# Performance work log

Measured on AMD Instinct MI355X. Metric: run time of the kernel, lower is better.

## Reference

```python
import jax, jax.numpy as jnp
import numpy as np

NUM_STAGES = 2
DE_NEIGHBORS = 3

def _square_distance(a, b):
    # a: [B,N,3], b: [B,S,3] -> [B,N,S] squared euclidean distances
    return (jnp.sum(a * a, axis=-1)[:, :, None]
            + jnp.sum(b * b, axis=-1)[:, None, :]
            - 2.0 * jnp.einsum('bnc,bsc->bns', a, b))

def _propagate(xyz1, xyz2, points1, points2, k):
    # xyz1:[B,N,3] fine, xyz2:[B,S,3] coarse, points1:[B,D1,N], points2:[B,D2,S]
    p2 = jnp.transpose(points2, (0, 2, 1))  # [B,S,D2]
    B, N, _ = xyz1.shape
    S = xyz2.shape[1]
    if S == 1:
        interp = jnp.broadcast_to(p2, (B, N, p2.shape[-1]))
    else:
        d = _square_distance(xyz1, xyz2)              # [B,N,S]
        neg_top, idx = jax.lax.top_k(-d, k)           # k smallest distances
        dists = -neg_top                              # [B,N,k]
        recip = 1.0 / (dists + 1e-8)
        weight = recip / jnp.sum(recip, axis=2, keepdims=True)  # [B,N,k]
        # gather neighbor features: [B,N,k,D2]
        gathered = jnp.take_along_axis(p2[:, None, :, :], idx[..., None], axis=2)
        interp = jnp.sum(gathered * weight[..., None], axis=2)  # [B,N,D2]
    if points1 is not None:
        p1 = jnp.transpose(points1, (0, 2, 1))        # [B,N,D1]
        new = jnp.concatenate([p1, interp], axis=-1)
    else:
        new = interp
    return jnp.transpose(new, (0, 2, 1))              # [B,D1+D2,N]

def setup_inputs() -> dict:
    key = jax.random.key(0)
    ks = jax.random.split(key, 6)
    return {
        'xyz0': jax.random.normal(ks[0], (4, 8192, 3), dtype=jnp.float32),
        'xyz1': jax.random.normal(ks[1], (4, 2048, 3), dtype=jnp.float32),
        'xyz2': jax.random.normal(ks[2], (4, 512, 3), dtype=jnp.float32),
        'x0': jax.random.normal(ks[3], (4, 128, 8192), dtype=jnp.float32),
        'x1': jax.random.normal(ks[4], (4, 256, 2048), dtype=jnp.float32),
        'x2': jax.random.normal(ks[5], (4, 512, 512), dtype=jnp.float32),
    }

def reference(xyz0, xyz1, xyz2, x0, x1, x2):
    # original forward reverses the lists; emulate with pre-reversed lists
    xyz_list = [xyz2, xyz1, xyz0]   # coarse -> fine
    x_list = [x2, x1, x0]
    x = x_list[0]
    for i in range(NUM_STAGES):
        x = _propagate(xyz_list[i + 1], xyz_list[i], x_list[i + 1], x, DE_NEIGHBORS)
    return x  # [4, 896, 8192]
```

## Files before the change

kernel.cpp:

```cpp
#include <hip/hip_runtime.h>

#define BIG 3.0e38f

typedef float vf4 __attribute__((ext_vector_type(4)));

__device__ __forceinline__ void insert3(float d, int s,
                                        float& d0, float& d1, float& d2,
                                        int& i0, int& i1, int& i2) {
    const bool b0 = d < d0;
    const bool b1 = d < d1;
    const bool b2 = d < d2;
    i2 = b1 ? i1 : (b2 ? s : i2);
    i1 = b0 ? i0 : (b1 ? s : i1);
    i0 = b0 ? s  : i0;
    const float nd1 = __builtin_amdgcn_fmed3f(d, d0, d1);
    d2 = __builtin_amdgcn_fmed3f(d, d1, d2);
    d0 = fminf(d, d0);
    d1 = nd1;
}

template <int S>
__device__ void knn_tile(const float* __restrict__ xyzF, const float* __restrict__ xyzC,
                         int N, int b, int nb,
                         int* __restrict__ idx, float* __restrict__ w,
                         void* smem) {
    constexpr int SPC = S / 8;
    float4* sc  = (float4*)smem;
    float*  smd = (float*)((char*)smem + S * 16);
    int*    smi = (int*)((char*)smem + S * 16 + 3072);
    const int tid = threadIdx.x;

    for (int i = tid; i < S; i += 256) {
        const float x = xyzC[(b * S + i) * 3 + 0];
        const float y = xyzC[(b * S + i) * 3 + 1];
        const float z = xyzC[(b * S + i) * 3 + 2];
        sc[i] = make_float4(x, y, z, x * x + y * y + z * z);
    }
    __syncthreads();

    const int q  = tid & 31;
    const int sp = tid >> 5;
    const int n  = nb + q;
    const float ax = xyzF[(b * N + n) * 3 + 0];
    const float ay = xyzF[(b * N + n) * 3 + 1];
    const float az = xyzF[(b * N + n) * 3 + 2];
    const float an = ax * ax + ay * ay + az * az;

    float d0 = BIG, d1 = BIG, d2 = BIG;
    int i0 = 0, i1 = 0, i2 = 0;
    const int s0 = sp * SPC;
#pragma unroll 8
    for (int s = s0; s < s0 + SPC; ++s) {
        const float4 p = sc[s];
        const float t = ax * p.x + ay * p.y + az * p.z;
        const float d = an + p.w - 2.0f * t;
        insert3(d, s, d0, d1, d2, i0, i1, i2);
    }

    smd[tid * 3 + 0] = d0; smi[tid * 3 + 0] = i0;
    smd[tid * 3 + 1] = d1; smi[tid * 3 + 1] = i1;
    smd[tid * 3 + 2] = d2; smi[tid * 3 + 2] = i2;
    __syncthreads();

    if (tid < 32) {
        float e0 = BIG, e1 = BIG, e2 = BIG;
        int j0 = 0, j1 = 0, j2 = 0;
#pragma unroll
        for (int ch = 0; ch < 8; ++ch) {
#pragma unroll
            for (int k = 0; k < 3; ++k) {
                insert3(smd[(ch * 32 + tid) * 3 + k], smi[(ch * 32 + tid) * 3 + k],
                        e0, e1, e2, j0, j1, j2);
            }
        }
        const float r0 = 1.0f / (e0 + 1e-8f);
        const float r1 = 1.0f / (e1 + 1e-8f);
        const float r2 = 1.0f / (e2 + 1e-8f);
        const float rs = r0 + r1 + r2;
        const int nn = nb + tid;
        idx[(b * 3 + 0) * N + nn] = j0;
        idx[(b * 3 + 1) * N + nn] = j1;
        idx[(b * 3 + 2) * N + nn] = j2;
        w[(b * 3 + 0) * N + nn] = r0 / rs;
        w[(b * 3 + 1) * N + nn] = r1 / rs;
        w[(b * 3 + 2) * N + nn] = r2 / rs;
    }
}

__device__ void transpose_tile(const float* __restrict__ in, float* __restrict__ out,
                               int C, int N, int OS,
                               int b, int nb, int cb, void* smem) {
    float (*s)[65] = (float (*)[65])smem;
    const int lo = threadIdx.x & 63;
    const int r  = threadIdx.x >> 6;
#pragma unroll
    for (int i = 0; i < 16; ++i) {
        const int cl = r + 4 * i;
        s[cl][lo] = in[((size_t)b * C + cb + cl) * N + nb + lo];
    }
    __syncthreads();
#pragma unroll
    for (int i = 0; i < 16; ++i) {
        const int pl = r + 4 * i;
        out[((size_t)b * N + nb + pl) * OS + cb + lo] = s[lo][pl];
    }
}

__global__ __launch_bounds__(256) void k1_stage(const float* __restrict__ xyz0,
                                                const float* __restrict__ xyz1,
                                                const float* __restrict__ xyz2,
                                                const float* __restrict__ x0,
                                                const float* __restrict__ x1,
                                                const float* __restrict__ x2,
                                                float* __restrict__ x1P,
                                                float* __restrict__ x2P,
                                                int* __restrict__ idx1,
                                                float* __restrict__ w1,
                                                int* __restrict__ idx2,
                                                float* __restrict__ w2,
                                                float* __restrict__ out) {
    __shared__ float4 smem4[2432];
    const int id = blockIdx.x;
    if (id < 1024) {
        const int b  = id >> 8;
        const int nb = (id & 255) * 32;
        knn_tile<2048>(xyz0, xyz1, 8192, b, nb, idx2, w2, smem4);
    } else if (id < 1280) {
        const int r  = id - 1024;
        const int b  = r >> 6;
        const int nb = (r & 63) * 32;
        knn_tile<512>(xyz1, xyz2, 2048, b, nb, idx1, w1, smem4);
    } else if (id < 1536) {
        const int r  = id - 1280;
        const int b  = r >> 6;
        const int nb = (r & 7) * 64;
        const int cb = ((r >> 3) & 7) * 64;
        transpose_tile(x2, x2P, 512, 512, 512, b, nb, cb, smem4);
    } else if (id < 2048) {
        const int r  = id - 1536;
        const int b  = r >> 7;
        const int nb = (r & 31) * 64;
        const int cb = ((r >> 5) & 3) * 64;
        transpose_tile(x1, x1P, 256, 2048, 256, b, nb, cb, smem4);
    } else {
        const int r  = id - 2048;
        const int b  = r >> 6;
        const int lb = r & 63;
        const vf4* src = (const vf4*)x0;
        vf4* dst = (vf4*)out;
#pragma unroll
        for (int t = 0; t < 16; ++t) {
            const int i = lb * 4096 + t * 256 + threadIdx.x;
            const vf4 v = __builtin_nontemporal_load(&src[(size_t)b * (128 * 2048) + i]);
            __builtin_nontemporal_store(v, &dst[(size_t)b * (896 * 2048) + i]);
        }
    }
}

__global__ __launch_bounds__(256) void final_unified(const float* __restrict__ x1P,
                                                     const float* __restrict__ x2P,
                                                     const int* __restrict__ idx1,
                                                     const float* __restrict__ w1,
                                                     const int* __restrict__ idx2,
                                                     const float* __restrict__ w2,
                                                     float* __restrict__ out) {
    __shared__ float tile[64][65];
    __shared__ int   sj1[3][64];
    __shared__ float sw1[3][64];
    __shared__ int   sj9[9][64];
    __shared__ float sw9[9][64];
    const int id  = blockIdx.x;
    const int xcd = id & 7;
    const int b   = xcd >> 1;
    const int ntile = ((id >> 3) << 1) | (xcd & 1);
    const int nb  = ntile * 64;
    const int tid = threadIdx.x;

    if (tid < 192) {
        const int p = tid & 63, k = tid >> 6;
        const int   j  = idx2[(b * 3 + k) * 8192 + nb + p];
        const float wk = w2[(b * 3 + k) * 8192 + nb + p];
        sj1[k][p] = j * 256;
        sw1[k][p] = wk;
#pragma unroll
        for (int m = 0; m < 3; ++m) {
            sj9[k * 3 + m][p] = idx1[(b * 3 + m) * 2048 + j] * 512;
            sw9[k * 3 + m][p] = wk * w1[(b * 3 + m) * 2048 + j];
        }
    }
    __syncthreads();

    const int c = tid & 63;
    const int r = tid >> 6;

    for (int ct = 0; ct < 4; ++ct) {
        const int cb = ct * 64;
        const float* xb = x1P + (size_t)b * 2048 * 256 + cb + c;
#pragma unroll 8
        for (int i = 0; i < 16; ++i) {
            const int p = r + 4 * i;
            tile[p][c] = sw1[0][p] * xb[sj1[0][p]]
                       + sw1[1][p] * xb[sj1[1][p]]
                       + sw1[2][p] * xb[sj1[2][p]];
        }
        __syncthreads();
        {
            const int p = tid & 63;
#pragma unroll
            for (int i = 0; i < 16; ++i) {
                const int cl = r + 4 * i;
                __builtin_nontemporal_store(tile[p][cl],
                    &out[((size_t)b * 896 + 128 + cb + cl) * 8192 + nb + p]);
            }
        }
        __syncthreads();
    }

    for (int ct = 0; ct < 8; ++ct) {
        const int cb = ct * 64;
        const float* xb = x2P + (size_t)b * 512 * 512 + cb + c;
#pragma unroll 4
        for (int i = 0; i < 16; ++i) {
            const int p = r + 4 * i;
            float v = 0.0f;
#pragma unroll
            for (int j = 0; j < 9; ++j) {
                v += sw9[j][p] * xb[sj9[j][p]];
            }
            tile[p][c] = v;
        }
        __syncthreads();
        {
            const int p = tid & 63;
#pragma unroll
            for (int i = 0; i < 16; ++i) {
                const int cl = r + 4 * i;
                __builtin_nontemporal_store(tile[p][cl],
                    &out[((size_t)b * 896 + 384 + cb + cl) * 8192 + nb + p]);
            }
        }
        __syncthreads();
    }
}

extern "C" void kernel_launch(void* const* d_in, const int* in_sizes, int n_in,
                              void* d_out, int out_size, void* d_ws, size_t ws_size,
                              hipStream_t stream) {
    const float* xyz0 = (const float*)d_in[0];
    const float* xyz1 = (const float*)d_in[1];
    const float* xyz2 = (const float*)d_in[2];
    const float* x0   = (const float*)d_in[3];
    const float* x1   = (const float*)d_in[4];
    const float* x2   = (const float*)d_in[5];
    float* out = (float*)d_out;

    char* ws = (char*)d_ws;
    float* x1P  = (float*)(ws + 0);
    float* x2P  = (float*)(ws + 8388608);
    int*   idx1 = (int*)(ws + 12582912);
    float* w1   = (float*)(ws + 12681216);
    int*   idx2 = (int*)(ws + 12779520);
    float* w2   = (float*)(ws + 13172736);

    k1_stage<<<dim3(2304), 256, 0, stream>>>(xyz0, xyz1, xyz2, x0, x1, x2,
                                             x1P, x2P, idx1, w1, idx2, w2, out);
    final_unified<<<dim3(512), 256, 0, stream>>>(x1P, x2P, idx1, w1, idx2, w2, out);
}
```

Baseline: 248.9 us.

## Rebalance work across two kernels with vectorized gathers and phased KNN tiles

Moves the x0 copy out of the first kernel into the second, so the first kernel only does KNN and transposes. The final gather kernel is split into many more independent blocks: the stage-2 gathers are spread over two channel halves per tile and the stage-1 gathers over one 64-channel slab each, and both now use float4 vector loads. The KNN is split into two phases over half of the coarse points to cut shared memory, and the distance uses a half-norm FMA form with the query norm added back at the end. A tie-breaking merge is used for the final top-3 selection. Together these aim at higher occupancy and better load balance, at the cost of recomputing the neighbor index and weight setup in every block and an extra barrier per KNN phase.

```diff
diff --git a/kernel.cpp b/kernel.cpp
--- a/kernel.cpp
+++ b/kernel.cpp
@@ -3,6 +3,8 @@
 #define BIG 3.0e38f
 
 typedef float vf4 __attribute__((ext_vector_type(4)));
+
+__device__ __forceinline__ vf4 ld4(const float* p) { return *(const vf4*)p; }
 
 __device__ __forceinline__ void insert3(float d, int s,
                                         float& d0, float& d1, float& d2,
@@ -19,42 +21,58 @@
     d1 = nd1;
 }
 
-template <int S>
+__device__ __forceinline__ void insert3_tie(float d, int s,
+                                            float& d0, float& d1, float& d2,
+                                            int& i0, int& i1, int& i2) {
+    const bool b0 = (d < d0) | ((d == d0) & (s < i0));
+    const bool b1 = (d < d1) | ((d == d1) & (s < i1));
+    const bool b2 = (d < d2) | ((d == d2) & (s < i2));
+    i2 = b1 ? i1 : (b2 ? s : i2);
+    i1 = b0 ? i0 : (b1 ? s : i1);
+    i0 = b0 ? s  : i0;
+    d2 = b1 ? d1 : (b2 ? d : d2);
+    d1 = b0 ? d0 : (b1 ? d : d1);
+    d0 = b0 ? d  : d0;
+}
+
+template <int S, int PHASES>
 __device__ void knn_tile(const float* __restrict__ xyzF, const float* __restrict__ xyzC,
                          int N, int b, int nb,
                          int* __restrict__ idx, float* __restrict__ w,
                          void* smem) {
-    constexpr int SPC = S / 8;
+    constexpr int H   = S / PHASES;
+    constexpr int SPC = H / 8;
     float4* sc  = (float4*)smem;
-    float*  smd = (float*)((char*)smem + S * 16);
-    int*    smi = (int*)((char*)smem + S * 16 + 3072);
+    float*  smd = (float*)((char*)smem + H * 16);
+    int*    smi = (int*)((char*)smem + H * 16 + 3072);
     const int tid = threadIdx.x;
-
-    for (int i = tid; i < S; i += 256) {
-        const float x = xyzC[(b * S + i) * 3 + 0];
-        const float y = xyzC[(b * S + i) * 3 + 1];
-        const float z = xyzC[(b * S + i) * 3 + 2];
-        sc[i] = make_float4(x, y, z, x * x + y * y + z * z);
-    }
-    __syncthreads();
-
-    const int q  = tid & 31;
-    const int sp = tid >> 5;
-    const int n  = nb + q;
+    const int q   = tid & 31;
+    const int sp  = tid >> 5;
+    const int n   = nb + q;
     const float ax = xyzF[(b * N + n) * 3 + 0];
     const float ay = xyzF[(b * N + n) * 3 + 1];
     const float az = xyzF[(b * N + n) * 3 + 2];
-    const float an = ax * ax + ay * ay + az * az;
 
     float d0 = BIG, d1 = BIG, d2 = BIG;
     int i0 = 0, i1 = 0, i2 = 0;
-    const int s0 = sp * SPC;
+
+    for (int ph = 0; ph < PHASES; ++ph) {
+        const int base = ph * H;
+        if (ph) __syncthreads();
+        for (int i = tid; i < H; i += 256) {
+            const float x = xyzC[(b * S + base + i) * 3 + 0];
+            const float y = xyzC[(b * S + base + i) * 3 + 1];
+            const float z = xyzC[(b * S + base + i) * 3 + 2];
+            sc[i] = make_float4(x, y, z, 0.5f * (x * x + y * y + z * z));
+        }
+        __syncthreads();
+        const int s0 = sp * SPC;
 #pragma unroll 8
-    for (int s = s0; s < s0 + SPC; ++s) {
-        const float4 p = sc[s];
-        const float t = ax * p.x + ay * p.y + az * p.z;
-        const float d = an + p.w - 2.0f * t;
-        insert3(d, s, d0, d1, d2, i0, i1, i2);
+        for (int t = 0; t < SPC; ++t) {
+            const float4 p = sc[s0 + t];
+            const float h = fmaf(-ax, p.x, fmaf(-ay, p.y, fmaf(-az, p.z, p.w)));
+            insert3(h, base + s0 + t, d0, d1, d2, i0, i1, i2);
+        }
     }
 
     smd[tid * 3 + 0] = d0; smi[tid * 3 + 0] = i0;
@@ -69,13 +87,14 @@
         for (int ch = 0; ch < 8; ++ch) {
 #pragma unroll
             for (int k = 0; k < 3; ++k) {
-                insert3(smd[(ch * 32 + tid) * 3 + k], smi[(ch * 32 + tid) * 3 + k],
-                        e0, e1, e2, j0, j1, j2);
-            }
-        }
-        const float r0 = 1.0f / (e0 + 1e-8f);
-        const float r1 = 1.0f / (e1 + 1e-8f);
-        const float r2 = 1.0f / (e2 + 1e-8f);
+                insert3_tie(smd[(ch * 32 + tid) * 3 + k], smi[(ch * 32 + tid) * 3 + k],
+                            e0, e1, e2, j0, j1, j2);
+            }
+        }
+        const float an = ax * ax + ay * ay + az * az;
+        const float r0 = 1.0f / (fmaf(2.0f, e0, an) + 1e-8f);
+        const float r1 = 1.0f / (fmaf(2.0f, e1, an) + 1e-8f);
+        const float r2 = 1.0f / (fmaf(2.0f, e2, an) + 1e-8f);
         const float rs = r0 + r1 + r2;
         const int nn = nb + tid;
         idx[(b * 3 + 0) * N + nn] = j0;
@@ -109,7 +128,6 @@
 __global__ __launch_bounds__(256) void k1_stage(const float* __restrict__ xyz0,
                                                 const float* __restrict__ xyz1,
                                                 const float* __restrict__ xyz2,
-                                                const float* __restrict__ x0,
                                                 const float* __restrict__ x1,
                                                 const float* __restrict__ x2,
                                                 float* __restrict__ x1P,
@@ -117,129 +135,144 @@
                                                 int* __restrict__ idx1,
                                                 float* __restrict__ w1,
                                                 int* __restrict__ idx2,
-                                                float* __restrict__ w2,
-                                                float* __restrict__ out) {
-    __shared__ float4 smem4[2432];
+                                                float* __restrict__ w2) {
+    __shared__ float4 smem4[1408];
     const int id = blockIdx.x;
     if (id < 1024) {
         const int b  = id >> 8;
         const int nb = (id & 255) * 32;
-        knn_tile<2048>(xyz0, xyz1, 8192, b, nb, idx2, w2, smem4);
+        knn_tile<2048, 2>(xyz0, xyz1, 8192, b, nb, idx2, w2, smem4);
     } else if (id < 1280) {
         const int r  = id - 1024;
         const int b  = r >> 6;
         const int nb = (r & 63) * 32;
-        knn_tile<512>(xyz1, xyz2, 2048, b, nb, idx1, w1, smem4);
+        knn_tile<512, 1>(xyz1, xyz2, 2048, b, nb, idx1, w1, smem4);
     } else if (id < 1536) {
         const int r  = id - 1280;
         const int b  = r >> 6;
         const int nb = (r & 7) * 64;
         const int cb = ((r >> 3) & 7) * 64;
         transpose_tile(x2, x2P, 512, 512, 512, b, nb, cb, smem4);
-    } else if (id < 2048) {
+    } else {
         const int r  = id - 1536;
         const int b  = r >> 7;
         const int nb = (r & 31) * 64;
         const int cb = ((r >> 5) & 3) * 64;
         transpose_tile(x1, x1P, 256, 2048, 256, b, nb, cb, smem4);
+    }
+}
+
+__global__ __launch_bounds__(256) void k2_final(const float* __restrict__ x0,
+                                                const float* __restrict__ x1P,
+                                                const float* __restrict__ x2P,
+                                                const int* __restrict__ idx1,
+                                                const float* __restrict__ w1,
+                                                const int* __restrict__ idx2,
+                                                const float* __restrict__ w2,
+                                                float* __restrict__ out) {
+    __shared__ vf4 smemv[1376];
+    float (*tile)[68] = (float (*)[68])smemv;
+    int*   sj9 = (int*)((float*)smemv + 4352);
+    float* sw9 = (float*)((float*)smemv + 4928);
+    const int id  = blockIdx.x;
+    const int tid = threadIdx.x;
+    const int q4  = tid & 15;
+    const int pg  = (tid >> 4) & 3;
+    const int r   = tid >> 6;
+
+    if (id < 1024) {
+        const int b     = id >> 8;
+        const int rem   = id & 255;
+        const int ntile = rem >> 1;
+        const int cq    = rem & 1;
+        const int nb    = ntile * 64;
+
+        if (tid < 192) {
+            const int p = tid & 63, k = tid >> 6;
+            const int   j  = idx2[(b * 3 + k) * 8192 + nb + p];
+            const float wk = w2[(b * 3 + k) * 8192 + nb + p];
+#pragma unroll
+            for (int m = 0; m < 3; ++m) {
+                sj9[(k * 3 + m) * 64 + p] = idx1[(b * 3 + m) * 2048 + j] * 512;
+                sw9[(k * 3 + m) * 64 + p] = wk * w1[(b * 3 + m) * 2048 + j];
+            }
+        }
+        __syncthreads();
+
+        for (int ct = 0; ct < 4; ++ct) {
+            const int cb = (cq * 4 + ct) * 64;
+            const float* xb = x2P + (size_t)b * 512 * 512 + cb + q4 * 4;
+#pragma unroll
+            for (int i = 0; i < 4; ++i) {
+                const int p = i * 16 + r * 4 + pg;
+                vf4 acc = sw9[0 * 64 + p] * ld4(xb + sj9[0 * 64 + p]);
+#pragma unroll
+                for (int j = 1; j < 9; ++j) {
+                    acc += sw9[j * 64 + p] * ld4(xb + sj9[j * 64 + p]);
+                }
+                *(vf4*)&tile[p][q4 * 4] = acc;
+            }
+            __syncthreads();
+            {
+                const int p2 = tid & 63;
+#pragma unroll
+                for (int i = 0; i < 16; ++i) {
+                    const int cl = r + 4 * i;
+                    __builtin_nontemporal_store(tile[p2][cl],
+                        &out[((size_t)b * 896 + 384 + cb + cl) * 8192 + nb + p2]);
+                }
+            }
+            __syncthreads();
+        }
+    } else if (id < 3072) {
+        const int t     = id - 1024;
+        const int b     = t >> 9;
+        const int rem   = t & 511;
+        const int ntile = rem >> 2;
+        const int ct    = rem & 3;
+        const int nb    = ntile * 64;
+        const int cb    = ct * 64;
+        int*   sj1 = sj9;
+        float* sw1 = sw9;
+
+        if (tid < 192) {
+            const int p = tid & 63, k = tid >> 6;
+            sj1[k * 64 + p] = idx2[(b * 3 + k) * 8192 + nb + p] * 256;
+            sw1[k * 64 + p] = w2[(b * 3 + k) * 8192 + nb + p];
+        }
+        __syncthreads();
+
+        const float* xb = x1P + (size_t)b * 2048 * 256 + cb + q4 * 4;
+#pragma unroll
+        for (int i = 0; i < 4; ++i) {
+            const int p = i * 16 + r * 4 + pg;
+            const vf4 acc = sw1[0 * 64 + p] * ld4(xb + sj1[0 * 64 + p])
+                          + sw1[1 * 64 + p] * ld4(xb + sj1[1 * 64 + p])
+                          + sw1[2 * 64 + p] * ld4(xb + sj1[2 * 64 + p]);
+            *(vf4*)&tile[p][q4 * 4] = acc;
+        }
+        __syncthreads();
+        {
+            const int p2 = tid & 63;
+#pragma unroll
+            for (int i = 0; i < 16; ++i) {
+                const int cl = r + 4 * i;
+                __builtin_nontemporal_store(tile[p2][cl],
+                    &out[((size_t)b * 896 + 128 + cb + cl) * 8192 + nb + p2]);
+            }
+        }
     } else {
-        const int r  = id - 2048;
-        const int b  = r >> 6;
-        const int lb = r & 63;
+        const int rr = id - 3072;
+        const int b  = rr >> 6;
+        const int lb = rr & 63;
         const vf4* src = (const vf4*)x0;
         vf4* dst = (vf4*)out;
 #pragma unroll
-        for (int t = 0; t < 16; ++t) {
-            const int i = lb * 4096 + t * 256 + threadIdx.x;
+        for (int t2 = 0; t2 < 16; ++t2) {
+            const int i = lb * 4096 + t2 * 256 + tid;
             const vf4 v = __builtin_nontemporal_load(&src[(size_t)b * (128 * 2048) + i]);
             __builtin_nontemporal_store(v, &dst[(size_t)b * (896 * 2048) + i]);
         }
-    }
-}
-
-__global__ __launch_bounds__(256) void final_unified(const float* __restrict__ x1P,
-                                                     const float* __restrict__ x2P,
-                                                     const int* __restrict__ idx1,
-                                                     const float* __restrict__ w1,
-                                                     const int* __restrict__ idx2,
-                                                     const float* __restrict__ w2,
-                                                     float* __restrict__ out) {
-    __shared__ float tile[64][65];
-    __shared__ int   sj1[3][64];
-    __shared__ float sw1[3][64];
-    __shared__ int   sj9[9][64];
-    __shared__ float sw9[9][64];
-    const int id  = blockIdx.x;
-    const int xcd = id & 7;
-    const int b   = xcd >> 1;
-    const int ntile = ((id >> 3) << 1) | (xcd & 1);
-    const int nb  = ntile * 64;
-    const int tid = threadIdx.x;
-
-    if (tid < 192) {
-        const int p = tid & 63, k = tid >> 6;
-        const int   j  = idx2[(b * 3 + k) * 8192 + nb + p];
-        const float wk = w2[(b * 3 + k) * 8192 + nb + p];
-        sj1[k][p] = j * 256;
-        sw1[k][p] = wk;
-#pragma unroll
-        for (int m = 0; m < 3; ++m) {
-            sj9[k * 3 + m][p] = idx1[(b * 3 + m) * 2048 + j] * 512;
-            sw9[k * 3 + m][p] = wk * w1[(b * 3 + m) * 2048 + j];
-        }
-    }
-    __syncthreads();
-
-    const int c = tid & 63;
-    const int r = tid >> 6;
-
-    for (int ct = 0; ct < 4; ++ct) {
-        const int cb = ct * 64;
-        const float* xb = x1P + (size_t)b * 2048 * 256 + cb + c;
-#pragma unroll 8
-        for (int i = 0; i < 16; ++i) {
-            const int p = r + 4 * i;
-            tile[p][c] = sw1[0][p] * xb[sj1[0][p]]
-                       + sw1[1][p] * xb[sj1[1][p]]
-                       + sw1[2][p] * xb[sj1[2][p]];
-        }
-        __syncthreads();
-        {
-            const int p = tid & 63;
-#pragma unroll
-            for (int i = 0; i < 16; ++i) {
-                const int cl = r + 4 * i;
-                __builtin_nontemporal_store(tile[p][cl],
-                    &out[((size_t)b * 896 + 128 + cb + cl) * 8192 + nb + p]);
-            }
-        }
-        __syncthreads();
-    }
-
-    for (int ct = 0; ct < 8; ++ct) {
-        const int cb = ct * 64;
-        const float* xb = x2P + (size_t)b * 512 * 512 + cb + c;
-#pragma unroll 4
-        for (int i = 0; i < 16; ++i) {
-            const int p = r + 4 * i;
-            float v = 0.0f;
-#pragma unroll
-            for (int j = 0; j < 9; ++j) {
-                v += sw9[j][p] * xb[sj9[j][p]];
-            }
-            tile[p][c] = v;
-        }
-        __syncthreads();
-        {
-            const int p = tid & 63;
-#pragma unroll
-            for (int i = 0; i < 16; ++i) {
-                const int cl = r + 4 * i;
-                __builtin_nontemporal_store(tile[p][cl],
-                    &out[((size_t)b * 896 + 384 + cb + cl) * 8192 + nb + p]);
-            }
-        }
-        __syncthreads();
     }
 }
 
@@ -262,7 +295,7 @@
     int*   idx2 = (int*)(ws + 12779520);
     float* w2   = (float*)(ws + 13172736);
 
-    k1_stage<<<dim3(2304), 256, 0, stream>>>(xyz0, xyz1, xyz2, x0, x1, x2,
-                                             x1P, x2P, idx1, w1, idx2, w2, out);
-    final_unified<<<dim3(512), 256, 0, stream>>>(x1P, x2P, idx1, w1, idx2, w2, out);
-}
+    k1_stage<<<dim3(2048), 256, 0, stream>>>(xyz0, xyz1, xyz2, x1, x2,
+                                             x1P, x2P, idx1, w1, idx2, w2);
+    k2_final<<<dim3(3328), 256, 0, stream>>>(x0, x1P, x2P, idx1, w1, idx2, w2, out);
+}
```

Measured after the change: 204.4 us. -17.9%, faster.
